# Kernel optimization log

Hardware: AMD Instinct MI355X
Metric: run time of the kernel (lower is better)

Reference implementation:

```python
import jax, jax.numpy as jnp
import numpy as np

N_QUBITS = 10
DIM = 768
N_LAYERS = 3
BATCH = 2048


def setup_inputs() -> dict:
    key = jax.random.key(0)
    ks = jax.random.split(key, 5)
    z_i = jax.random.normal(ks[0], (BATCH, DIM), jnp.float32)
    W_in = jax.random.normal(ks[1], (DIM, N_QUBITS), jnp.float32) / np.sqrt(DIM).astype(np.float32)
    b_in = jnp.zeros((N_QUBITS,), jnp.float32)
    # torch.rand(shape) * pi  -> uniform [0, pi)
    weights = jax.random.uniform(ks[2], (N_LAYERS, N_QUBITS, 3), jnp.float32) * np.float32(np.pi)
    W_out = jax.random.normal(ks[3], (N_QUBITS, DIM), jnp.float32) / np.sqrt(N_QUBITS).astype(np.float32)
    b_out = jnp.zeros((DIM,), jnp.float32)
    return {"z_i": z_i, "W_in": W_in, "b_in": b_in, "weights": weights, "W_out": W_out, "b_out": b_out}


def _apply_gate(state, gate, q):
    """Apply a 1-qubit gate on wire q (wire 0 = most significant bit, PennyLane order).
    state: (B, 2**n) complex64; gate: (2,2) shared or (B,2,2) per-sample."""
    B, dim = state.shape
    left = 2 ** q
    right = dim // (2 * left)
    s = state.reshape(B, left, 2, right)
    eq = 'bij,bkjl->bkil' if gate.ndim == 3 else 'ij,bkjl->bkil'
    return jnp.einsum(eq, gate, s).reshape(B, dim)


def _apply_cnot(state, c, t, n):
    B = state.shape[0]
    s = state.reshape((B,) + (2,) * n)
    s = jnp.moveaxis(s, (1 + c, 1 + t), (1, 2))
    # control=1 block: flip target bit
    s = jnp.concatenate([s[:, :1], s[:, 1:, ::-1]], axis=1)
    s = jnp.moveaxis(s, (1, 2), (1 + c, 1 + t))
    return s.reshape(B, -1)


def _circuit(angles, weights):
    """AngleEmbedding (RX) + StronglyEntanglingLayers (Rot + ring of CNOTs), PauliZ expvals."""
    B, n = angles.shape
    L = weights.shape[0]
    state = jnp.zeros((B, 2 ** n), jnp.complex64).at[:, 0].set(1.0)
    # AngleEmbedding: RX(a) = [[cos(a/2), -i sin(a/2)], [-i sin(a/2), cos(a/2)]], per sample
    half = (0.5 * angles).astype(jnp.complex64)
    c = jnp.cos(half)
    s = -1j * jnp.sin(half)
    for q in range(n):
        g = jnp.stack([jnp.stack([c[:, q], s[:, q]], -1),
                       jnp.stack([s[:, q], c[:, q]], -1)], -2)  # (B,2,2)
        state = _apply_gate(state, g, q)
    wc = weights.astype(jnp.complex64)
    for l in range(L):
        for q in range(n):
            phi, theta, omega = wc[l, q, 0], wc[l, q, 1], wc[l, q, 2]
            ct = jnp.cos(0.5 * theta)
            st = jnp.sin(0.5 * theta)
            # Rot(phi,theta,omega) = RZ(omega) RY(theta) RZ(phi)
            g = jnp.stack([
                jnp.stack([jnp.exp(-0.5j * (phi + omega)) * ct, -jnp.exp(0.5j * (phi - omega)) * st]),
                jnp.stack([jnp.exp(-0.5j * (phi - omega)) * st, jnp.exp(0.5j * (phi + omega)) * ct]),
            ])
            state = _apply_gate(state, g, q)
        r = (l % (n - 1)) + 1  # PennyLane default ranges
        for i in range(n):
            state = _apply_cnot(state, i, (i + r) % n, n)
    probs = (state.real ** 2 + state.imag ** 2).reshape((B,) + (2,) * n)
    evs = []
    for w in range(n):
        axes = tuple(a for a in range(1, n + 1) if a != 1 + w)
        pw = probs.sum(axes)  # (B, 2)
        evs.append(pw[:, 0] - pw[:, 1])  # <Z_w>
    return jnp.stack(evs, -1)  # (B, n) float32


def reference(z_i, W_in, b_in, weights, W_out, b_out):
    # torch code detaches the projected angles before the qnode (.cpu().detach())
    angles = jax.lax.stop_gradient(z_i @ W_in + b_in)  # (B, n_qubits)
    evs = _circuit(angles, weights)
    return evs @ W_out + b_out  # (B, classical_input_dim)
```

## Files before the change

kernel.cpp:

```cpp
#include <hip/hip_runtime.h>

typedef float f2 __attribute__((ext_vector_type(2)));

constexpr int NQ   = 10;
constexpr int CDIM = 768;
constexpr int NL   = 3;
constexpr int NREG = 16;
constexpr int WPB  = 4;


template<int CTRL>
__device__ __forceinline__ float dppmov(float x) {
    return __int_as_float(__builtin_amdgcn_update_dpp(
        __float_as_int(x), __float_as_int(x), CTRL, 0xF, 0xF, true));
}

template<int MASK>
__device__ __forceinline__ float lxor(float x, int lane) {
    static_assert(MASK == 1 || MASK == 2 || MASK == 4 || MASK == 8, "");
    if constexpr (MASK == 1)      return dppmov<0xB1>(x);
    else if constexpr (MASK == 2) return dppmov<0x4E>(x);
    else if constexpr (MASK == 4) {
        const float a = dppmov<0x104>(x);
        const float b = dppmov<0x114>(x);
        return ((lane >> 2) & 1) ? b : a;
    }
    else                          return dppmov<0x128>(x);
}

template<int B>
__device__ __forceinline__ void swap2(float x, float& lo, float& hi) {
    const unsigned xu = __float_as_uint(x);
#if __has_builtin(__builtin_amdgcn_permlane16_swap) && __has_builtin(__builtin_amdgcn_permlane32_swap)
    if constexpr (B == 4) {
        auto r = __builtin_amdgcn_permlane16_swap(xu, xu, false, false);
        lo = __uint_as_float(r[0]); hi = __uint_as_float(r[1]);
    } else {
        auto r = __builtin_amdgcn_permlane32_swap(xu, xu, false, false);
        lo = __uint_as_float(r[0]); hi = __uint_as_float(r[1]);
    }
#else
    float d, s;
    if constexpr (B == 4)
        asm("v_mov_b32 %0, %2\n\tv_mov_b32 %1, %2\n\ts_nop 1\n\t"
            "v_permlane16_swap_b32 %0, %1"
            : "=&v"(d), "=&v"(s) : "v"(x));
    else
        asm("v_mov_b32 %0, %2\n\tv_mov_b32 %1, %2\n\ts_nop 1\n\t"
            "v_permlane32_swap_b32 %0, %1"
            : "=&v"(d), "=&v"(s) : "v"(x));
    lo = d; hi = s;
#endif
}

__device__ __forceinline__ float wave_sum(float v) {
    v += dppmov<0xB1>(v);
    v += dppmov<0x4E>(v);
    v += dppmov<0x141>(v);
    v += dppmov<0x140>(v);
    float lo, hi;
    swap2<4>(v, lo, hi); v = lo + hi;
    swap2<5>(v, lo, hi); v = lo + hi;
    return v;
}


__device__ __forceinline__ f2 swapneg(f2 b) { f2 r; r.x = -b.y; r.y = b.x; return r; }
__device__ __forceinline__ f2 cmul(f2 a, f2 b) { return b * a.x + swapneg(b) * a.y; }
__device__ __forceinline__ f2 cfma(f2 a, f2 b, f2 acc) { return acc + b * a.x + swapneg(b) * a.y; }


template<int B>
__device__ __forceinline__ void gate_bit(f2 (&v)[NREG], int lane,
                                         f2 g00, f2 g01, f2 g10, f2 g11) {
    if constexpr (B >= 6) {
        constexpr int rb = B - 6;
#pragma unroll
        for (int p = 0; p < NREG / 2; ++p) {
            const int r0 = ((p >> rb) << (rb + 1)) | (p & ((1 << rb) - 1));
            const int r1 = r0 | (1 << rb);
            const f2 a0 = v[r0], a1 = v[r1];
            v[r0] = cfma(g01, a1, cmul(g00, a0));
            v[r1] = cfma(g11, a1, cmul(g10, a0));
        }
    } else if constexpr (B >= 4) {
        const bool hb = (lane >> B) & 1;
        const f2 A  = hb ? g10 : g00;
        const f2 Bc = hb ? g11 : g01;
#pragma unroll
        for (int r = 0; r < NREG; ++r) {
            float lx, hx, ly, hy;
            swap2<B>(v[r].x, lx, hx);
            swap2<B>(v[r].y, ly, hy);
            f2 lo; lo.x = lx; lo.y = ly;
            f2 hi; hi.x = hx; hi.y = hy;
            v[r] = cfma(Bc, hi, cmul(A, lo));
        }
    } else {
        const bool hb = (lane >> B) & 1;
        const f2 cO = hb ? g11 : g00;
        const f2 cP = hb ? g10 : g01;
#pragma unroll
        for (int r = 0; r < NREG; ++r) {
            f2 p;
            p.x = lxor<(1 << B)>(v[r].x, lane);
            p.y = lxor<(1 << B)>(v[r].y, lane);
            v[r] = cfma(cP, p, cmul(cO, v[r]));
        }
    }
}

template<int BT>
__device__ __forceinline__ float partner(float x, int lane) {
    if constexpr (BT >= 4) {
        float lo, hi; swap2<BT>(x, lo, hi);
        return ((lane >> BT) & 1) ? lo : hi;
    } else return lxor<(1 << BT)>(x, lane);
}


template<int BC, int BT>
__device__ __forceinline__ void cnot(f2 (&v)[NREG], int lane) {
    if constexpr (BC >= 6 && BT >= 6) {
        constexpr int rc = BC - 6, rt = BT - 6;
#pragma unroll
        for (int r = 0; r < NREG; ++r)
            if (((r >> rc) & 1) && !((r >> rt) & 1)) {
                const int r1 = r | (1 << rt);
                const f2 t = v[r]; v[r] = v[r1]; v[r1] = t;
            }
    } else if constexpr (BC >= 6) {
        constexpr int rc = BC - 6;
#pragma unroll
        for (int r = 0; r < NREG; ++r)
            if ((r >> rc) & 1) {
                f2 n;
                n.x = partner<BT>(v[r].x, lane);
                n.y = partner<BT>(v[r].y, lane);
                v[r] = n;
            }
    } else if constexpr (BT >= 6) {
        constexpr int rt = BT - 6;
        const bool c = (lane >> BC) & 1;
#pragma unroll
        for (int p = 0; p < NREG / 2; ++p) {
            const int r0 = ((p >> rt) << (rt + 1)) | (p & ((1 << rt) - 1));
            const int r1 = r0 | (1 << rt);
            const f2 a = v[r0], b = v[r1];
            v[r0] = c ? b : a;
            v[r1] = c ? a : b;
        }
    } else {
        const bool c = (lane >> BC) & 1;
#pragma unroll
        for (int r = 0; r < NREG; ++r) {
            f2 n;
            n.x = c ? partner<BT>(v[r].x, lane) : v[r].x;
            n.y = c ? partner<BT>(v[r].y, lane) : v[r].y;
            v[r] = n;
        }
    }
}


template<int Q = 0>
__device__ __forceinline__ void rot_layer_q(f2 (&v)[NREG], int lane,
                                            const float* __restrict__ w30) {
    if constexpr (Q < NQ) {
        const float phi = w30[Q * 3 + 0];
        const float th  = w30[Q * 3 + 1];
        const float om  = w30[Q * 3 + 2];
        float st, ct, sA, cA, sB, cB;
        __sincosf(0.5f * th, &st, &ct);
        __sincosf(0.5f * (phi + om), &sA, &cA);
        __sincosf(0.5f * (phi - om), &sB, &cB);
        f2 g00 = { ct * cA, -ct * sA};
        f2 g01 = {-st * cB, -st * sB};
        f2 g10 = { st * cB, -st * sB};
        f2 g11 = { ct * cA,  ct * sA};
        gate_bit<9 - Q>(v, lane, g00, g01, g10, g11);
        rot_layer_q<Q + 1>(v, lane, w30);
    }
}

template<int L, int I = 0>
__device__ __forceinline__ void cnot_ring(f2 (&v)[NREG], int lane) {
    if constexpr (I < NQ) {
        constexpr int R = (L % (NQ - 1)) + 1;
        cnot<9 - I, 9 - ((I + R) % NQ)>(v, lane);
        cnot_ring<L, I + 1>(v, lane);
    }
}

constexpr unsigned ring2_mask(int w) {
    unsigned M[NQ] = {};
    for (int i = 0; i < NQ; ++i) M[i] = 1u << (9 - i);
    for (int i = 0; i < NQ; ++i) M[(i + 3) % NQ] ^= M[i];
    return M[w];
}

template<unsigned MR>
__device__ __forceinline__ float regsum16(const float (&pr)[NREG]) {
    float s = 0.f;
#pragma unroll
    for (int r = 0; r < NREG; ++r)
        s = (__builtin_popcount((unsigned)r & MR) & 1) ? s - pr[r] : s + pr[r];
    return s;
}

template<int W = 0>
__device__ __forceinline__ void measure_all(const float (&pr)[NREG], int lane,
                                            float (&ev)[NQ]) {
    if constexpr (W < NQ) {
        constexpr unsigned m  = ring2_mask(W);
        constexpr unsigned mr = (m >> 6) & 0xFu;
        constexpr unsigned ml = m & 63u;
        float s = regsum16<mr>(pr);
        if constexpr (ml != 0) {
            const unsigned flip = (unsigned)((__popc(lane & (int)ml) & 1)) << 31;
            s = __uint_as_float(__float_as_uint(s) ^ flip);
        }
        ev[W] = wave_sum(s);
        measure_all<W + 1>(pr, lane, ev);
    }
}

__global__ __launch_bounds__(64 * WPB, 2) void qembed(
    const float* __restrict__ z,
    const float* __restrict__ Win,
    const float* __restrict__ bin,
    const float* __restrict__ wts,
    const float* __restrict__ Wout,
    const float* __restrict__ bout,
    float* __restrict__ out)
{
    const int wave = threadIdx.x >> 6;
    const int lane = threadIdx.x & 63;
    const int samp = blockIdx.x * WPB + wave;

    float ang[NQ];
    {
        const float* zrow = z + (size_t)samp * CDIM;
        float zr[CDIM / 64];
#pragma unroll
        for (int j = 0; j < CDIM / 64; ++j) zr[j] = zrow[lane + j * 64];

        f2 a5[NQ / 2];
#pragma unroll
        for (int h = 0; h < NQ / 2; ++h) a5[h] = (f2){0.f, 0.f};
#pragma unroll
        for (int j = 0; j < CDIM / 64; ++j) {
            const int k = lane + j * 64;
            const f2* wr = (const f2*)(Win + k * NQ);
#pragma unroll
            for (int h = 0; h < NQ / 2; ++h) a5[h] += wr[h] * zr[j];
        }
#pragma unroll
        for (int h = 0; h < NQ / 2; ++h) {
            ang[2 * h]     = wave_sum(a5[h].x) + bin[2 * h];
            ang[2 * h + 1] = wave_sum(a5[h].y) + bin[2 * h + 1];
        }
    }

    f2 f0[NQ], f1[NQ];
#pragma unroll
    for (int q = 0; q < NQ; ++q) {
        const float phi = wts[q * 3 + 0];
        const float th  = wts[q * 3 + 1];
        const float om  = wts[q * 3 + 2];
        float st, ct, sA, cA, sB, cB, s, c;
        __sincosf(0.5f * th, &st, &ct);
        __sincosf(0.5f * (phi + om), &sA, &cA);
        __sincosf(0.5f * (phi - om), &sB, &cB);
        __sincosf(0.5f * ang[q], &s, &c);
        const float g00x =  ct * cA, g00y = -ct * sA;
        const float g01x = -st * cB, g01y = -st * sB;
        const float g10x =  st * cB, g10y = -st * sB;
        const float g11x =  ct * cA, g11y =  ct * sA;
        f2 a, b;
        a.x = g00x * c + s * g01y;  a.y = g00y * c - s * g01x;
        b.x = g10x * c + s * g11y;  b.y = g10y * c - s * g11x;
        f0[q] = a; f1[q] = b;
    }

    const int gray = lane ^ (lane >> 1);
    const int l0 = lane & 1;
    const int l5 = (lane >> 5) & 1;
    f2 G0 = ((gray >> 0) & 1) ? f1[9] : f0[9];
    f2 G1 = ((gray >> 1) & 1) ? f1[8] : f0[8];
    f2 G2 = ((gray >> 2) & 1) ? f1[7] : f0[7];
    f2 G3 = ((gray >> 3) & 1) ? f1[6] : f0[6];
    f2 G4 = ((gray >> 4) & 1) ? f1[5] : f0[5];
    const f2 L5 = cmul(cmul(G0, G1), cmul(G2, cmul(G3, G4)));
    f2 B5[2];
    B5[0] = l5 ? f1[4] : f0[4];
    B5[1] = l5 ? f0[4] : f1[4];
    f2 D8[2], E9[2];
    D8[0] = l0 ? f1[1] : f0[1];
    D8[1] = l0 ? f0[1] : f1[1];
    E9[0] = l0 ? f1[0] : f0[0];
    E9[1] = l0 ? f0[0] : f1[0];

    f2 P1[2];
    P1[0] = cmul(L5, B5[0]);
    P1[1] = cmul(L5, B5[1]);
    f2 P2[4];
#pragma unroll
    for (int r1b = 0; r1b < 2; ++r1b)
#pragma unroll
        for (int r0b = 0; r0b < 2; ++r0b)
            P2[r0b + 2 * r1b] = cmul(P1[r0b], (r0b ^ r1b) ? f1[3] : f0[3]);
    f2 P3[8];
#pragma unroll
    for (int r2b = 0; r2b < 2; ++r2b)
#pragma unroll
        for (int p = 0; p < 4; ++p)
            P3[p + 4 * r2b] = cmul(P2[p], (((p >> 1) & 1) ^ r2b) ? f1[2] : f0[2]);
    f2 W[4];
#pragma unroll
    for (int d = 0; d < 2; ++d)
#pragma unroll
        for (int u = 0; u < 2; ++u)
            W[u + 2 * d] = cmul(D8[u], E9[d]);

    f2 v[NREG];
#pragma unroll
    for (int r = 0; r < NREG; ++r) {
        const int r2b = (r >> 2) & 1, r3b = (r >> 3) & 1;
        v[r] = cmul(P3[r & 7], W[(r2b ^ r3b) + 2 * r3b]);
    }

#pragma unroll 1
    for (int l = 1; l < NL; ++l) {
        rot_layer_q(v, lane, wts + l * NQ * 3);
        if (l == 1) cnot_ring<1>(v, lane);
    }

    float pr[NREG];
#pragma unroll
    for (int r = 0; r < NREG; ++r) pr[r] = v[r].x * v[r].x + v[r].y * v[r].y;

    float ev[NQ];
    measure_all(pr, lane, ev);

#pragma unroll
    for (int half = 0; half < 2; ++half) {
        float wr[6][NQ];
        float bo[6];
#pragma unroll
        for (int j = 0; j < 6; ++j) {
            const int d = lane + (half * 6 + j) * 64;
            bo[j] = bout[d];
#pragma unroll
            for (int q = 0; q < NQ; ++q) wr[j][q] = Wout[q * CDIM + d];
        }
#pragma unroll
        for (int j = 0; j < 6; ++j) {
            const int d = lane + (half * 6 + j) * 64;
            float o = bo[j];
#pragma unroll
            for (int q = 0; q < NQ; ++q) o += ev[q] * wr[j][q];
            out[(size_t)samp * CDIM + d] = o;
        }
    }
}

extern "C" void kernel_launch(void* const* d_in, const int* in_sizes, int n_in,
                              void* d_out, int out_size, void* d_ws, size_t ws_size,
                              hipStream_t stream) {
    const float* z    = (const float*)d_in[0];
    const float* Win  = (const float*)d_in[1];
    const float* bin  = (const float*)d_in[2];
    const float* wts  = (const float*)d_in[3];
    const float* Wout = (const float*)d_in[4];
    const float* bout = (const float*)d_in[5];
    float* outp       = (float*)d_out;

    const int batch  = in_sizes[0] / CDIM;
    const int blocks = batch / WPB;
    qembed<<<blocks, 64 * WPB, 0, stream>>>(z, Win, bin, wts, Wout, bout, outp);
}
```

Measured before the change: 29.04 us.

## Precompute rotation gates in LDS, vectorize z loads, rechunk output loop

The layer 1 and 2 rotation gate matrices are now computed once per block by 20 threads and stored in shared memory. Previously every lane recomputed the sincos values for every gate. The z row is loaded as float4, which changes the per-lane k mapping for W_in accesses, and the output projection is split into three non-unrolled chunks of four columns instead of two unrolled halves of six. The cost is an added __syncthreads, LDS reads in the gate loop, and possibly less ILP in the output stage, with lower register pressure in return.

```diff
diff --git a/kernel.cpp b/kernel.cpp
--- a/kernel.cpp
+++ b/kernel.cpp
@@ -164,22 +164,15 @@
 
 
 template<int Q = 0>
-__device__ __forceinline__ void rot_layer_q(f2 (&v)[NREG], int lane,
-                                            const float* __restrict__ w30) {
+__device__ __forceinline__ void rot_layer_lds(f2 (&v)[NREG], int lane,
+                                              const float4* g ) {
     if constexpr (Q < NQ) {
-        const float phi = w30[Q * 3 + 0];
-        const float th  = w30[Q * 3 + 1];
-        const float om  = w30[Q * 3 + 2];
-        float st, ct, sA, cA, sB, cB;
-        __sincosf(0.5f * th, &st, &ct);
-        __sincosf(0.5f * (phi + om), &sA, &cA);
-        __sincosf(0.5f * (phi - om), &sB, &cB);
-        f2 g00 = { ct * cA, -ct * sA};
-        f2 g01 = {-st * cB, -st * sB};
-        f2 g10 = { st * cB, -st * sB};
-        f2 g11 = { ct * cA,  ct * sA};
+        const float4 p0 = g[Q * 2];
+        const float4 p1 = g[Q * 2 + 1];
+        f2 g00 = {p0.x, p0.y}, g01 = {p0.z, p0.w};
+        f2 g10 = {p1.x, p1.y}, g11 = {p1.z, p1.w};
         gate_bit<9 - Q>(v, lane, g00, g01, g10, g11);
-        rot_layer_q<Q + 1>(v, lane, w30);
+        rot_layer_lds<Q + 1>(v, lane, g);
     }
 }
 
@@ -234,26 +227,44 @@
     const float* __restrict__ bout,
     float* __restrict__ out)
 {
+    __shared__ float4 gl4[2][NQ][2];
+
     const int wave = threadIdx.x >> 6;
     const int lane = threadIdx.x & 63;
     const int samp = blockIdx.x * WPB + wave;
 
+    if (threadIdx.x < 2 * NQ) {
+        const int li = threadIdx.x / NQ, q = threadIdx.x % NQ;
+        const float* wp = wts + ((li + 1) * NQ + q) * 3;
+        const float phi = wp[0], th = wp[1], om = wp[2];
+        float st, ct, sA, cA, sB, cB;
+        __sincosf(0.5f * th, &st, &ct);
+        __sincosf(0.5f * (phi + om), &sA, &cA);
+        __sincosf(0.5f * (phi - om), &sB, &cB);
+        gl4[li][q][0] = make_float4( ct * cA, -ct * sA, -st * cB, -st * sB);
+        gl4[li][q][1] = make_float4( st * cB, -st * sB,  ct * cA,  ct * sA);
+    }
+
     float ang[NQ];
     {
-        const float* zrow = z + (size_t)samp * CDIM;
-        float zr[CDIM / 64];
-#pragma unroll
-        for (int j = 0; j < CDIM / 64; ++j) zr[j] = zrow[lane + j * 64];
+        const float4* z4 = (const float4*)(z + (size_t)samp * CDIM);
+        float4 zr[3];
+#pragma unroll
+        for (int j = 0; j < 3; ++j) zr[j] = z4[lane + j * 64];
 
         f2 a5[NQ / 2];
 #pragma unroll
         for (int h = 0; h < NQ / 2; ++h) a5[h] = (f2){0.f, 0.f};
 #pragma unroll
-        for (int j = 0; j < CDIM / 64; ++j) {
-            const int k = lane + j * 64;
-            const f2* wr = (const f2*)(Win + k * NQ);
-#pragma unroll
-            for (int h = 0; h < NQ / 2; ++h) a5[h] += wr[h] * zr[j];
+        for (int j = 0; j < 3; ++j) {
+            const float zc[4] = {zr[j].x, zr[j].y, zr[j].z, zr[j].w};
+#pragma unroll
+            for (int c = 0; c < 4; ++c) {
+                const int k = 4 * (lane + j * 64) + c;
+                const f2* wr = (const f2*)(Win + k * NQ);
+#pragma unroll
+                for (int h = 0; h < NQ / 2; ++h) a5[h] += wr[h] * zc[c];
+            }
         }
 #pragma unroll
         for (int h = 0; h < NQ / 2; ++h) {
@@ -330,10 +341,12 @@
         v[r] = cmul(P3[r & 7], W[(r2b ^ r3b) + 2 * r3b]);
     }
 
+    __syncthreads();
+
 #pragma unroll 1
-    for (int l = 1; l < NL; ++l) {
-        rot_layer_q(v, lane, wts + l * NQ * 3);
-        if (l == 1) cnot_ring<1>(v, lane);
+    for (int l = 0; l < 2; ++l) {
+        rot_layer_lds(v, lane, &gl4[l][0][0]);
+        if (l == 0) cnot_ring<1>(v, lane);
     }
 
     float pr[NREG];
@@ -343,20 +356,20 @@
     float ev[NQ];
     measure_all(pr, lane, ev);
 
-#pragma unroll
-    for (int half = 0; half < 2; ++half) {
-        float wr[6][NQ];
-        float bo[6];
-#pragma unroll
-        for (int j = 0; j < 6; ++j) {
-            const int d = lane + (half * 6 + j) * 64;
+#pragma unroll 1
+    for (int ch = 0; ch < 3; ++ch) {
+        float wr[4][NQ];
+        float bo[4];
+#pragma unroll
+        for (int j = 0; j < 4; ++j) {
+            const int d = lane + (ch * 4 + j) * 64;
             bo[j] = bout[d];
 #pragma unroll
             for (int q = 0; q < NQ; ++q) wr[j][q] = Wout[q * CDIM + d];
         }
 #pragma unroll
-        for (int j = 0; j < 6; ++j) {
-            const int d = lane + (half * 6 + j) * 64;
+        for (int j = 0; j < 4; ++j) {
+            const int d = lane + (ch * 4 + j) * 64;
             float o = bo[j];
 #pragma unroll
             for (int q = 0; q < NQ; ++q) o += ev[q] * wr[j][q];
```

New measurement: 27.45 us. 1.06x faster.
